# Kernel tuning notes

Hardware: AMD Instinct MI355X
Metric: run time of the kernel (lower is better)

Reference implementation:

```python
import jax, jax.numpy as jnp
import numpy as np

T, B, F, H = 1024, 128, 243, 20  # timesteps, batch, feature dim, hidden dim
POOL = 4  # MaxPool1d(4, 4) over the 512 channel axis -> 128


def setup_inputs() -> dict:
    key = jax.random.key(0)
    ks = jax.random.split(key, 9)
    s = lambda fan_in: 1.0 / np.sqrt(fan_in)
    return {
        "feats": jax.random.normal(ks[0], (T, B * POOL, F), dtype=jnp.float32),
        "e0": jax.random.normal(ks[1], (B, H), dtype=jnp.float32),
        # PyTorch GRUCell params: gates stacked as [r; z; n]
        "W_ih": jax.random.uniform(ks[2], (3 * H, F), jnp.float32, -s(H), s(H)),
        "W_hh": jax.random.uniform(ks[3], (3 * H, H), jnp.float32, -s(H), s(H)),
        "b_ih": jax.random.uniform(ks[4], (3 * H,), jnp.float32, -s(H), s(H)),
        "b_hh": jax.random.uniform(ks[5], (3 * H,), jnp.float32, -s(H), s(H)),
        # decoder: Linear(20, 243) + ReLU
        "W_dec": jax.random.uniform(ks[6], (F, H), jnp.float32, -s(H), s(H)),
        "b_dec": jax.random.uniform(ks[7], (F,), jnp.float32, -s(H), s(H)),
    }


def reference(feats, e0, W_ih, W_hh, b_ih, b_hh, W_dec, b_dec):
    # temporal max-pool over the 512 axis (kernel=4, stride=4) -> [T, B, F]
    h_seq = feats.reshape(T, B, POOL, F).max(axis=2)
    # precompute input-gate projections once (vectorized over T): [T, B, 3H]
    x_gates = jnp.einsum('tbf,gf->tbg', h_seq, W_ih) + b_ih

    def step(e, inp):
        h_t, xg = inp
        hg = e @ W_hh.T + b_hh
        xr, xz, xn = jnp.split(xg, 3, axis=-1)
        hr, hz, hn = jnp.split(hg, 3, axis=-1)
        r = jax.nn.sigmoid(xr + hr)
        z = jax.nn.sigmoid(xz + hz)
        n = jnp.tanh(xn + r * hn)
        e_new = (1.0 - z) * n + z * e
        fo = jax.nn.relu(e_new @ W_dec.T + b_dec)
        loss = jnp.mean((fo - h_t) ** 2)
        return e_new, loss

    _, losses = jax.lax.scan(step, e0, (h_seq, x_gates))
    return jnp.mean(losses)  # sum(loss_list) / step
```

## Files before the change

kernel.cpp:

```cpp
#include <hip/hip_runtime.h>
#include <cstddef>

#define T_ 1024
#define B_ 128
#define F_ 243
#define H_ 20
#define G_ 60
#define R_ 512
#define P_ 8
#define FP_ 256
#define HS_ 244

__device__ __forceinline__ float rdlane(float v, int l) {
  return __int_as_float(__builtin_amdgcn_readlane(__float_as_int(v), l));
}
#define RCP(x) __builtin_amdgcn_rcpf(x)
#if __has_builtin(__builtin_amdgcn_exp2f)
#define EXP2(x) __builtin_amdgcn_exp2f(x)
#else
#define EXP2(x) __expf((x) * 0.6931471805599453f)
#endif
#define NL2E_ -1.4426950408889634f
#define L2E2_ 2.8853900817779268f

__global__ __launch_bounds__(256) void k1a_pool(
    const float* __restrict__ feats, float* __restrict__ h_seq,
    const float* __restrict__ W_ih, float* __restrict__ Wt)
{
  const int bid = blockIdx.x;
  if (bid < 60) {
    const int i = bid * 256 + threadIdx.x;
    if (i < FP_ * G_) {
      const int f = i / G_, g = i - f * G_;
      Wt[(size_t)f * G_ + g] = (f < F_) ? W_ih[(size_t)g * F_ + f] : 0.f;
    }
  }
  const int t = bid & (T_ - 1);
  const int b0 = (bid >> 10) << 3;
  const int col = threadIdx.x;
  if (col < F_) {
    #pragma unroll
    for (int bb = 0; bb < 8; ++bb) {
      const float* p =
          feats + ((size_t)t * R_ + (size_t)(b0 + bb) * 4) * F_ + col;
      const float v =
          fmaxf(fmaxf(p[0], p[F_]), fmaxf(p[2 * F_], p[3 * F_]));
      h_seq[((size_t)(b0 + bb) * T_ + t) * HS_ + col] = v;
    }
  }
}

__global__ __launch_bounds__(256) void k1b_gemm(
    const float* __restrict__ h_seq, const float* __restrict__ Wt,
    const float* __restrict__ b_ih, float* __restrict__ xg)
{
  __shared__ __align__(16) float Ws[64 * 60];
  const int bid = blockIdx.x;
  const int b = bid >> 4;
  const int t0 = (bid & 15) << 6;
  const int tid = threadIdx.x;
  const int rg = tid >> 4;
  const int gcol = tid & 15;
  const int gc4 = (gcol < 15) ? gcol * 4 : 56;
  const float* hsb = h_seq + ((size_t)b * T_ + t0) * HS_;

  float acc[4][4];
  #pragma unroll
  for (int i = 0; i < 4; ++i)
    #pragma unroll
    for (int j = 0; j < 4; ++j) acc[i][j] = 0.f;

  for (int c = 0; c < 4; ++c) {
    const int FC = c * 64;
    __syncthreads();
    for (int j = tid; j < 64 * 60; j += 256)
      Ws[j] = Wt[(size_t)FC * G_ + j];
    __syncthreads();
    #pragma unroll
    for (int fj = 0; fj < 16; ++fj) {
      const float* wp = &Ws[(fj * 4) * 60 + gc4];
      const float4 w0 = *(const float4*)(wp);
      const float4 w1 = *(const float4*)(wp + 60);
      const float4 w2 = *(const float4*)(wp + 120);
      const float4 w3 = *(const float4*)(wp + 180);
      #pragma unroll
      for (int i = 0; i < 4; ++i) {
        const int row = (rg << 2) + i;
        const float4 a4 =
            *(const float4*)&hsb[(size_t)row * HS_ + FC + fj * 4];
        acc[i][0] = fmaf(a4.x, w0.x, fmaf(a4.y, w1.x, fmaf(a4.z, w2.x, fmaf(a4.w, w3.x, acc[i][0]))));
        acc[i][1] = fmaf(a4.x, w0.y, fmaf(a4.y, w1.y, fmaf(a4.z, w2.y, fmaf(a4.w, w3.y, acc[i][1]))));
        acc[i][2] = fmaf(a4.x, w0.z, fmaf(a4.y, w1.z, fmaf(a4.z, w2.z, fmaf(a4.w, w3.z, acc[i][2]))));
        acc[i][3] = fmaf(a4.x, w0.w, fmaf(a4.y, w1.w, fmaf(a4.z, w2.w, fmaf(a4.w, w3.w, acc[i][3]))));
      }
    }
  }

  if (gcol < 15) {
    const float4 bi4 = *(const float4*)&b_ih[gc4];
    #pragma unroll
    for (int i = 0; i < 4; ++i) {
      const int row = (rg << 2) + i;
      float4 o;
      o.x = acc[i][0] + bi4.x;  o.y = acc[i][1] + bi4.y;
      o.z = acc[i][2] + bi4.z;  o.w = acc[i][3] + bi4.w;
      *(float4*)&xg[((size_t)b * T_ + t0 + row) * G_ + gc4] = o;
    }
  }
}

__global__ __launch_bounds__(320) void k2_fused(
    const float* __restrict__ e0, const float* __restrict__ W_hh,
    const float* __restrict__ b_hh, const float* __restrict__ xg,
    const float* __restrict__ h_seq, const float* __restrict__ W_dec,
    const float* __restrict__ b_dec, float* __restrict__ partials)
{
  __shared__ float ebuf[2][P_][H_];
  __shared__ float red[8];
  const int b = blockIdx.x;
  const int tid = threadIdx.x;
  const int lane = tid & 63;
  const int wave = tid >> 6;
  float acc = 0.f;

  if (wave == 0) {
    const bool own = lane < H_;
    const int j0 = own ? lane : 0;

    float2 wr2[10], wz2[10], wn2[10];
    #pragma unroll
    for (int k = 0; k < 10; ++k) {
      const float2 a = *(const float2*)&W_hh[j0 * H_ + 2 * k];
      const float2 c = *(const float2*)&W_hh[(j0 + 20) * H_ + 2 * k];
      const float2 d = *(const float2*)&W_hh[(j0 + 40) * H_ + 2 * k];
      wr2[k] = make_float2(a.x * NL2E_, a.y * NL2E_);
      wz2[k] = make_float2(c.x * NL2E_, c.y * NL2E_);
      wn2[k] = make_float2(d.x * L2E2_, d.y * L2E2_);
    }
    const float bhr = b_hh[j0] * NL2E_;
    const float bhz = b_hh[j0 + 20] * NL2E_;
    const float bhn = b_hh[j0 + 40] * L2E2_;

    float e_own = e0[b * H_ + j0];
    float2 es2[10];
    #pragma unroll
    for (int k = 0; k < 10; ++k) {
      es2[k].x = rdlane(e_own, 2 * k);
      es2[k].y = rdlane(e_own, 2 * k + 1);
    }

    const float* xgb = xg + (size_t)b * T_ * G_;
    float xr[P_], xz[P_], xn[P_];
    #pragma unroll
    for (int j = 0; j < P_; ++j) {
      xr[j] = xgb[(size_t)j * G_ + j0] * NL2E_;
      xz[j] = xgb[(size_t)j * G_ + j0 + 20] * NL2E_;
      xn[j] = xgb[(size_t)j * G_ + j0 + 40] * L2E2_;
    }

#define STEP(j, RELOAD)                                                    \
    {                                                                      \
      const int t = t0 + (j);                                              \
      const float xrv = xr[j], xzv = xz[j], xnv = xn[j];                   \
      if (RELOAD) {                                                        \
        const float* xp = xgb + (size_t)(t + P_) * G_;                     \
        xr[j] = xp[j0] * NL2E_;                                            \
        xz[j] = xp[j0 + 20] * NL2E_;                                       \
        xn[j] = xp[j0 + 40] * L2E2_;                                       \
      }                                                                    \
      float2 rA = make_float2(bhr, 0.f), rB = make_float2(0.f, 0.f);       \
      float2 zA = make_float2(bhz, 0.f), zB = make_float2(0.f, 0.f);       \
      float2 nA = make_float2(bhn, 0.f), nB = make_float2(0.f, 0.f);       \
      _Pragma("unroll")                                                    \
      for (int k = 0; k < 5; ++k) {                                        \
        rA = wr2[k] * es2[k] + rA;   rB = wr2[k + 5] * es2[k + 5] + rB;    \
        zA = wz2[k] * es2[k] + zA;   zB = wz2[k + 5] * es2[k + 5] + zB;    \
        nA = wn2[k] * es2[k] + nA;   nB = wn2[k + 5] * es2[k + 5] + nB;    \
      }                                                                    \
      const float hr2 = (rA.x + rB.x) + (rA.y + rB.y);                     \
      const float hz2 = (zA.x + zB.x) + (zA.y + zB.y);                     \
      const float hn2 = (nA.x + nB.x) + (nA.y + nB.y);                     \
      const float rg = RCP(1.f + EXP2(xrv + hr2));                         \
      const float zg = RCP(1.f + EXP2(xzv + hz2));                         \
      const float aa2 = fmaf(rg, hn2, xnv);                                \
      const float ng = fmaf(-2.f, RCP(EXP2(aa2) + 1.f), 1.f);              \
      const float enew = fmaf(zg, e_own - ng, ng);                         \
      if (own) ebuf[(t0 >> 3) & 1][j][lane] = enew;                        \
      e_own = enew;                                                        \
      _Pragma("unroll")                                                    \
      for (int k = 0; k < 10; ++k) {                                       \
        es2[k].x = rdlane(enew, 2 * k);                                    \
        es2[k].y = rdlane(enew, 2 * k + 1);                                \
      }                                                                    \
    }

    for (int t0 = 0; t0 < T_ - P_; t0 += P_) {
      STEP(0, true) STEP(1, true) STEP(2, true) STEP(3, true)
      STEP(4, true) STEP(5, true) STEP(6, true) STEP(7, true)
      __syncthreads();
    }
    {
      const int t0 = T_ - P_;
      STEP(0, false) STEP(1, false) STEP(2, false) STEP(3, false)
      STEP(4, false) STEP(5, false) STEP(6, false) STEP(7, false)
      __syncthreads();
    }
#undef STEP
  } else {
    const int ct = tid - 64;
    const bool act = ct < F_;
    const int f = act ? ct : 0;
    float wd[H_];
    #pragma unroll
    for (int k = 0; k < H_; ++k) wd[k] = W_dec[f * H_ + k];
    const float bd = b_dec[f];
    const float* hsb = h_seq + (size_t)b * T_ * HS_;

    float hcur[P_], hnxt[P_];
    #pragma unroll
    for (int j = 0; j < P_; ++j) hcur[j] = hsb[(size_t)j * HS_ + f];

    for (int g = 0; g < T_ / P_; ++g) {
      __syncthreads();
      if (g < T_ / P_ - 1) {
        #pragma unroll
        for (int j = 0; j < P_; ++j)
          hnxt[j] = hsb[(size_t)(P_ * (g + 1) + j) * HS_ + f];
      }
      const float* eb = &ebuf[g & 1][0][0];
      #pragma unroll
      for (int j = 0; j < P_; ++j) {
        const float2* ep = (const float2*)&eb[j * H_];
        float d = bd;
        #pragma unroll
        for (int k = 0; k < 10; ++k) {
          const float2 e2 = ep[k];
          d = fmaf(wd[2 * k], e2.x, fmaf(wd[2 * k + 1], e2.y, d));
        }
        const float fo = fmaxf(d, 0.f);
        const float df = fo - hcur[j];
        if (act) acc = fmaf(df, df, acc);
      }
      #pragma unroll
      for (int j = 0; j < P_; ++j) hcur[j] = hnxt[j];
    }
  }

  #pragma unroll
  for (int m = 32; m >= 1; m >>= 1) acc += __shfl_xor(acc, m);
  if (lane == 0) red[wave] = acc;
  __syncthreads();
  if (tid == 0)
    partials[b] = ((red[0] + red[1]) + (red[2] + red[3])) + red[4];
}

__global__ __launch_bounds__(64) void k3_reduce(
    const float* __restrict__ partials, float* __restrict__ out)
{
  const int lane = threadIdx.x;
  float a = partials[lane] + partials[lane + 64];
  #pragma unroll
  for (int m = 32; m >= 1; m >>= 1) a += __shfl_xor(a, m);
  if (lane == 0) out[0] = a * (float)(1.0 / ((double)T_ * B_ * F_));
}

extern "C" void kernel_launch(void* const* d_in, const int* in_sizes, int n_in,
                              void* d_out, int out_size, void* d_ws, size_t ws_size,
                              hipStream_t stream) {
  const float* feats = (const float*)d_in[0];
  const float* e0    = (const float*)d_in[1];
  const float* W_ih  = (const float*)d_in[2];
  const float* W_hh  = (const float*)d_in[3];
  const float* b_ih  = (const float*)d_in[4];
  const float* b_hh  = (const float*)d_in[5];
  const float* W_dec = (const float*)d_in[6];
  const float* b_dec = (const float*)d_in[7];
  float* out = (float*)d_out;

  float* ws = (float*)d_ws;
  float* h_seq    = ws;
  float* xgates   = ws + (size_t)B_ * T_ * HS_;
  float* partials = xgates + (size_t)B_ * T_ * G_;
  float* Wt       = partials + 128;

  hipLaunchKernelGGL(k1a_pool, dim3(T_ * (B_ / 8)), dim3(256), 0, stream,
                     feats, h_seq, W_ih, Wt);
  hipLaunchKernelGGL(k1b_gemm, dim3(B_ * 16), dim3(256), 0, stream,
                     h_seq, Wt, b_ih, xgates);
  hipLaunchKernelGGL(k2_fused, dim3(B_), dim3(320), 0, stream,
                     e0, W_hh, b_hh, xgates, h_seq, W_dec, b_dec, partials);
  hipLaunchKernelGGL(k3_reduce, dim3(1), dim3(64), 0, stream,
                     partials, out);
}
```

Before: 445.5 us.

## Fuse input-gate GEMM into recurrent kernel, pipelined via shared-memory double buffer

Removes the separate input-projection GEMM kernel and its global xgates buffer. The four decoder waves of the recurrent kernel now compute the gate projections for the next group of 8 timesteps from h_seq and a shared-memory copy of W_ih, writing them into a double-buffered LDS tile. The recurrent wave then reads them from LDS. This saves a launch and global traffic, but puts the GEMM work on only 128 blocks, and that work must keep pace with the serial recurrence.

```diff
diff --git a/kernel.cpp b/kernel.cpp
--- a/kernel.cpp
+++ b/kernel.cpp
@@ -8,6 +8,7 @@
 #define G_ 60
 #define R_ 512
 #define P_ 8
+#define NG_ (T_ / P_)
 #define FP_ 256
 #define HS_ 244
 
@@ -50,78 +51,26 @@
   }
 }
 
-__global__ __launch_bounds__(256) void k1b_gemm(
-    const float* __restrict__ h_seq, const float* __restrict__ Wt,
-    const float* __restrict__ b_ih, float* __restrict__ xg)
+__global__ __launch_bounds__(320) void k2_mega(
+    const float* __restrict__ e0, const float* __restrict__ W_hh,
+    const float* __restrict__ b_hh, const float* __restrict__ Wt,
+    const float* __restrict__ b_ih, const float* __restrict__ h_seq,
+    const float* __restrict__ W_dec, const float* __restrict__ b_dec,
+    float* __restrict__ partials)
 {
-  __shared__ __align__(16) float Ws[64 * 60];
-  const int bid = blockIdx.x;
-  const int b = bid >> 4;
-  const int t0 = (bid & 15) << 6;
-  const int tid = threadIdx.x;
-  const int rg = tid >> 4;
-  const int gcol = tid & 15;
-  const int gc4 = (gcol < 15) ? gcol * 4 : 56;
-  const float* hsb = h_seq + ((size_t)b * T_ + t0) * HS_;
-
-  float acc[4][4];
-  #pragma unroll
-  for (int i = 0; i < 4; ++i)
-    #pragma unroll
-    for (int j = 0; j < 4; ++j) acc[i][j] = 0.f;
-
-  for (int c = 0; c < 4; ++c) {
-    const int FC = c * 64;
-    __syncthreads();
-    for (int j = tid; j < 64 * 60; j += 256)
-      Ws[j] = Wt[(size_t)FC * G_ + j];
-    __syncthreads();
-    #pragma unroll
-    for (int fj = 0; fj < 16; ++fj) {
-      const float* wp = &Ws[(fj * 4) * 60 + gc4];
-      const float4 w0 = *(const float4*)(wp);
-      const float4 w1 = *(const float4*)(wp + 60);
-      const float4 w2 = *(const float4*)(wp + 120);
-      const float4 w3 = *(const float4*)(wp + 180);
-      #pragma unroll
-      for (int i = 0; i < 4; ++i) {
-        const int row = (rg << 2) + i;
-        const float4 a4 =
-            *(const float4*)&hsb[(size_t)row * HS_ + FC + fj * 4];
-        acc[i][0] = fmaf(a4.x, w0.x, fmaf(a4.y, w1.x, fmaf(a4.z, w2.x, fmaf(a4.w, w3.x, acc[i][0]))));
-        acc[i][1] = fmaf(a4.x, w0.y, fmaf(a4.y, w1.y, fmaf(a4.z, w2.y, fmaf(a4.w, w3.y, acc[i][1]))));
-        acc[i][2] = fmaf(a4.x, w0.z, fmaf(a4.y, w1.z, fmaf(a4.z, w2.z, fmaf(a4.w, w3.z, acc[i][2]))));
-        acc[i][3] = fmaf(a4.x, w0.w, fmaf(a4.y, w1.w, fmaf(a4.z, w2.w, fmaf(a4.w, w3.w, acc[i][3]))));
-      }
-    }
-  }
-
-  if (gcol < 15) {
-    const float4 bi4 = *(const float4*)&b_ih[gc4];
-    #pragma unroll
-    for (int i = 0; i < 4; ++i) {
-      const int row = (rg << 2) + i;
-      float4 o;
-      o.x = acc[i][0] + bi4.x;  o.y = acc[i][1] + bi4.y;
-      o.z = acc[i][2] + bi4.z;  o.w = acc[i][3] + bi4.w;
-      *(float4*)&xg[((size_t)b * T_ + t0 + row) * G_ + gc4] = o;
-    }
-  }
-}
-
-__global__ __launch_bounds__(320) void k2_fused(
-    const float* __restrict__ e0, const float* __restrict__ W_hh,
-    const float* __restrict__ b_hh, const float* __restrict__ xg,
-    const float* __restrict__ h_seq, const float* __restrict__ W_dec,
-    const float* __restrict__ b_dec, float* __restrict__ partials)
-{
+  __shared__ __align__(16) float Ws[244 * 60];
+  __shared__ float xgbuf[2][P_][G_];
   __shared__ float ebuf[2][P_][H_];
   __shared__ float red[8];
   const int b = blockIdx.x;
   const int tid = threadIdx.x;
   const int lane = tid & 63;
   const int wave = tid >> 6;
+  const float* hsb = h_seq + (size_t)b * T_ * HS_;
   float acc = 0.f;
+
+  for (int i = tid; i < 244 * 60; i += 320) Ws[i] = Wt[i];
+  __syncthreads();
 
   if (wave == 0) {
     const bool own = lane < H_;
@@ -148,26 +97,13 @@
       es2[k].x = rdlane(e_own, 2 * k);
       es2[k].y = rdlane(e_own, 2 * k + 1);
     }
-
-    const float* xgb = xg + (size_t)b * T_ * G_;
+    __syncthreads();
+
     float xr[P_], xz[P_], xn[P_];
-    #pragma unroll
-    for (int j = 0; j < P_; ++j) {
-      xr[j] = xgb[(size_t)j * G_ + j0] * NL2E_;
-      xz[j] = xgb[(size_t)j * G_ + j0 + 20] * NL2E_;
-      xn[j] = xgb[(size_t)j * G_ + j0 + 40] * L2E2_;
-    }
-
-#define STEP(j, RELOAD)                                                    \
+
+#define STEP(j)                                                            \
     {                                                                      \
-      const int t = t0 + (j);                                              \
       const float xrv = xr[j], xzv = xz[j], xnv = xn[j];                   \
-      if (RELOAD) {                                                        \
-        const float* xp = xgb + (size_t)(t + P_) * G_;                     \
-        xr[j] = xp[j0] * NL2E_;                                            \
-        xz[j] = xp[j0 + 20] * NL2E_;                                       \
-        xn[j] = xp[j0 + 40] * L2E2_;                                       \
-      }                                                                    \
       float2 rA = make_float2(bhr, 0.f), rB = make_float2(0.f, 0.f);       \
       float2 zA = make_float2(bhz, 0.f), zB = make_float2(0.f, 0.f);       \
       float2 nA = make_float2(bhn, 0.f), nB = make_float2(0.f, 0.f);       \
@@ -185,7 +121,7 @@
       const float aa2 = fmaf(rg, hn2, xnv);                                \
       const float ng = fmaf(-2.f, RCP(EXP2(aa2) + 1.f), 1.f);              \
       const float enew = fmaf(zg, e_own - ng, ng);                         \
-      if (own) ebuf[(t0 >> 3) & 1][j][lane] = enew;                        \
+      if (own) ebuf[m & 1][j][lane] = enew;                                \
       e_own = enew;                                                        \
       _Pragma("unroll")                                                    \
       for (int k = 0; k < 10; ++k) {                                       \
@@ -194,56 +130,93 @@
       }                                                                    \
     }
 
-    for (int t0 = 0; t0 < T_ - P_; t0 += P_) {
-      STEP(0, true) STEP(1, true) STEP(2, true) STEP(3, true)
-      STEP(4, true) STEP(5, true) STEP(6, true) STEP(7, true)
+    for (int m = 0; m < NG_; ++m) {
+      const float* xb = &xgbuf[m & 1][0][0];
+      #pragma unroll
+      for (int j = 0; j < P_; ++j) {
+        xr[j] = xb[j * G_ + j0];
+        xz[j] = xb[j * G_ + j0 + 20];
+        xn[j] = xb[j * G_ + j0 + 40];
+      }
+      STEP(0) STEP(1) STEP(2) STEP(3) STEP(4) STEP(5) STEP(6) STEP(7)
       __syncthreads();
     }
-    {
-      const int t0 = T_ - P_;
-      STEP(0, false) STEP(1, false) STEP(2, false) STEP(3, false)
-      STEP(4, false) STEP(5, false) STEP(6, false) STEP(7, false)
-      __syncthreads();
-    }
+    __syncthreads();
 #undef STEP
   } else {
     const int ct = tid - 64;
+    const int rr = ct >> 5;
+    const int q = ct & 31;
+    const bool qact = q < 30;
     const bool act = ct < F_;
     const int f = act ? ct : 0;
+
     float wd[H_];
     #pragma unroll
     for (int k = 0; k < H_; ++k) wd[k] = W_dec[f * H_ + k];
     const float bd = b_dec[f];
-    const float* hsb = h_seq + (size_t)b * T_ * HS_;
-
+
+    float2 sc2 = make_float2(0.f, 0.f), bs2 = make_float2(0.f, 0.f);
+    if (qact) {
+      const float s = (q < 20) ? NL2E_ : L2E2_;
+      sc2 = make_float2(s, s);
+      bs2 = make_float2(b_ih[2 * q] * s, b_ih[2 * q + 1] * s);
+    }
+
+#define GEMM_GRP(GRP, BUF)                                                 \
+    if (qact) {                                                            \
+      const float* hrow = hsb + (size_t)((GRP) * P_ + rr) * HS_;           \
+      float2 aE = make_float2(0.f, 0.f), aO = make_float2(0.f, 0.f);       \
+      _Pragma("unroll 4")                                                  \
+      for (int f4 = 0; f4 < 61; ++f4) {                                    \
+        const float4 h4 = *(const float4*)&hrow[f4 * 4];                   \
+        const float2 u0 = *(const float2*)&Ws[(f4 * 4 + 0) * 60 + 2 * q];  \
+        const float2 u1 = *(const float2*)&Ws[(f4 * 4 + 1) * 60 + 2 * q];  \
+        const float2 u2 = *(const float2*)&Ws[(f4 * 4 + 2) * 60 + 2 * q];  \
+        const float2 u3 = *(const float2*)&Ws[(f4 * 4 + 3) * 60 + 2 * q];  \
+        aE = u0 * make_float2(h4.x, h4.x) + aE;                            \
+        aO = u1 * make_float2(h4.y, h4.y) + aO;                            \
+        aE = u2 * make_float2(h4.z, h4.z) + aE;                            \
+        aO = u3 * make_float2(h4.w, h4.w) + aO;                            \
+      }                                                                    \
+      const float2 a2 = (aE + aO) * sc2 + bs2;                             \
+      *(float2*)&xgbuf[BUF][rr][2 * q] = a2;                               \
+    }
+
+    GEMM_GRP(0, 0)
     float hcur[P_], hnxt[P_];
     #pragma unroll
     for (int j = 0; j < P_; ++j) hcur[j] = hsb[(size_t)j * HS_ + f];
-
-    for (int g = 0; g < T_ / P_; ++g) {
-      __syncthreads();
-      if (g < T_ / P_ - 1) {
+    __syncthreads();
+
+    for (int m = 0; m <= NG_; ++m) {
+      if (m >= 1 && m < NG_) {
         #pragma unroll
         for (int j = 0; j < P_; ++j)
-          hnxt[j] = hsb[(size_t)(P_ * (g + 1) + j) * HS_ + f];
+          hnxt[j] = hsb[(size_t)(P_ * m + j) * HS_ + f];
       }
-      const float* eb = &ebuf[g & 1][0][0];
-      #pragma unroll
-      for (int j = 0; j < P_; ++j) {
-        const float2* ep = (const float2*)&eb[j * H_];
-        float d = bd;
+      if (m <= NG_ - 2) GEMM_GRP(m + 1, (m + 1) & 1)
+      if (m >= 1) {
+        const float* eb = &ebuf[(m - 1) & 1][0][0];
         #pragma unroll
-        for (int k = 0; k < 10; ++k) {
-          const float2 e2 = ep[k];
-          d = fmaf(wd[2 * k], e2.x, fmaf(wd[2 * k + 1], e2.y, d));
+        for (int j = 0; j < P_; ++j) {
+          const float2* ep = (const float2*)&eb[j * H_];
+          float d = bd;
+          #pragma unroll
+          for (int k = 0; k < 10; ++k) {
+            const float2 e2 = ep[k];
+            d = fmaf(wd[2 * k], e2.x, fmaf(wd[2 * k + 1], e2.y, d));
+          }
+          const float fo = fmaxf(d, 0.f);
+          const float df = fo - hcur[j];
+          if (act) acc = fmaf(df, df, acc);
         }
-        const float fo = fmaxf(d, 0.f);
-        const float df = fo - hcur[j];
-        if (act) acc = fmaf(df, df, acc);
+        #pragma unroll
+        for (int j = 0; j < P_; ++j) hcur[j] = hnxt[j];
       }
-      #pragma unroll
-      for (int j = 0; j < P_; ++j) hcur[j] = hnxt[j];
-    }
+      __syncthreads();
+    }
+#undef GEMM_GRP
   }
 
   #pragma unroll
@@ -279,16 +252,13 @@
 
   float* ws = (float*)d_ws;
   float* h_seq    = ws;
-  float* xgates   = ws + (size_t)B_ * T_ * HS_;
-  float* partials = xgates + (size_t)B_ * T_ * G_;
-  float* Wt       = partials + 128;
+  float* Wt       = ws + (size_t)B_ * T_ * HS_;
+  float* partials = Wt + (size_t)FP_ * G_;
 
   hipLaunchKernelGGL(k1a_pool, dim3(T_ * (B_ / 8)), dim3(256), 0, stream,
                      feats, h_seq, W_ih, Wt);
-  hipLaunchKernelGGL(k1b_gemm, dim3(B_ * 16), dim3(256), 0, stream,
-                     h_seq, Wt, b_ih, xgates);
-  hipLaunchKernelGGL(k2_fused, dim3(B_), dim3(320), 0, stream,
-                     e0, W_hh, b_hh, xgates, h_seq, W_dec, b_dec, partials);
+  hipLaunchKernelGGL(k2_mega, dim3(B_), dim3(320), 0, stream,
+                     e0, W_hh, b_hh, Wt, b_ih, h_seq, W_dec, b_dec, partials);
   hipLaunchKernelGGL(k3_reduce, dim3(1), dim3(64), 0, stream,
                      partials, out);
 }
```

Result: slower. 1.612 ms (+261.8%).

## Process two batch rows per recurrent block to interleave independent GRU chains

Applied to the files above, without the earlier changes.

The fused recurrence kernel now handles two batch elements per block. The single recurrent wave interleaves the two independent GRU dependency chains, and eight decoder waves (two rows of 256 threads) consume a doubled shared buffer. This is meant to hide the serial latency of each step by giving the recurrent wave independent instructions to overlap, while halving the grid to 64 blocks. The cost is longer per-step instruction streams, more register pressure in wave 0, and fewer blocks on a GPU with many compute units.

```diff
diff --git a/kernel.cpp b/kernel.cpp
--- a/kernel.cpp
+++ b/kernel.cpp
@@ -109,14 +109,14 @@
   }
 }
 
-__global__ __launch_bounds__(320) void k2_fused(
+__global__ __launch_bounds__(576) void k2_fused(
     const float* __restrict__ e0, const float* __restrict__ W_hh,
     const float* __restrict__ b_hh, const float* __restrict__ xg,
     const float* __restrict__ h_seq, const float* __restrict__ W_dec,
     const float* __restrict__ b_dec, float* __restrict__ partials)
 {
-  __shared__ float ebuf[2][P_][H_];
-  __shared__ float red[8];
+  __shared__ float ebuf[2][2][P_][H_];
+  __shared__ float red[12];
   const int b = blockIdx.x;
   const int tid = threadIdx.x;
   const int lane = tid & 63;
@@ -141,56 +141,83 @@
     const float bhz = b_hh[j0 + 20] * NL2E_;
     const float bhn = b_hh[j0 + 40] * L2E2_;
 
-    float e_own = e0[b * H_ + j0];
-    float2 es2[10];
+    float eA = e0[(2 * b) * H_ + j0];
+    float eB = e0[(2 * b + 1) * H_ + j0];
+    float2 esA[10], esB[10];
     #pragma unroll
     for (int k = 0; k < 10; ++k) {
-      es2[k].x = rdlane(e_own, 2 * k);
-      es2[k].y = rdlane(e_own, 2 * k + 1);
-    }
-
-    const float* xgb = xg + (size_t)b * T_ * G_;
-    float xr[P_], xz[P_], xn[P_];
+      esA[k].x = rdlane(eA, 2 * k);  esA[k].y = rdlane(eA, 2 * k + 1);
+      esB[k].x = rdlane(eB, 2 * k);  esB[k].y = rdlane(eB, 2 * k + 1);
+    }
+
+    const float* xgbA = xg + (size_t)(2 * b) * T_ * G_;
+    const float* xgbB = xg + (size_t)(2 * b + 1) * T_ * G_;
+    float xrA[P_], xzA[P_], xnA[P_], xrB[P_], xzB[P_], xnB[P_];
     #pragma unroll
     for (int j = 0; j < P_; ++j) {
-      xr[j] = xgb[(size_t)j * G_ + j0] * NL2E_;
-      xz[j] = xgb[(size_t)j * G_ + j0 + 20] * NL2E_;
-      xn[j] = xgb[(size_t)j * G_ + j0 + 40] * L2E2_;
+      xrA[j] = xgbA[(size_t)j * G_ + j0] * NL2E_;
+      xzA[j] = xgbA[(size_t)j * G_ + j0 + 20] * NL2E_;
+      xnA[j] = xgbA[(size_t)j * G_ + j0 + 40] * L2E2_;
+      xrB[j] = xgbB[(size_t)j * G_ + j0] * NL2E_;
+      xzB[j] = xgbB[(size_t)j * G_ + j0 + 20] * NL2E_;
+      xnB[j] = xgbB[(size_t)j * G_ + j0 + 40] * L2E2_;
     }
 
 #define STEP(j, RELOAD)                                                    \
     {                                                                      \
       const int t = t0 + (j);                                              \
-      const float xrv = xr[j], xzv = xz[j], xnv = xn[j];                   \
+      const float xrvA = xrA[j], xzvA = xzA[j], xnvA = xnA[j];             \
+      const float xrvB = xrB[j], xzvB = xzB[j], xnvB = xnB[j];             \
       if (RELOAD) {                                                        \
-        const float* xp = xgb + (size_t)(t + P_) * G_;                     \
-        xr[j] = xp[j0] * NL2E_;                                            \
-        xz[j] = xp[j0 + 20] * NL2E_;                                       \
-        xn[j] = xp[j0 + 40] * L2E2_;                                       \
+        const float* xpA = xgbA + (size_t)(t + P_) * G_;                   \
+        const float* xpB = xgbB + (size_t)(t + P_) * G_;                   \
+        xrA[j] = xpA[j0] * NL2E_;       xrB[j] = xpB[j0] * NL2E_;          \
+        xzA[j] = xpA[j0 + 20] * NL2E_;  xzB[j] = xpB[j0 + 20] * NL2E_;     \
+        xnA[j] = xpA[j0 + 40] * L2E2_;  xnB[j] = xpB[j0 + 40] * L2E2_;     \
       }                                                                    \
-      float2 rA = make_float2(bhr, 0.f), rB = make_float2(0.f, 0.f);       \
-      float2 zA = make_float2(bhz, 0.f), zB = make_float2(0.f, 0.f);       \
-      float2 nA = make_float2(bhn, 0.f), nB = make_float2(0.f, 0.f);       \
+      float2 r0A = make_float2(bhr, 0.f), r1A = make_float2(0.f, 0.f);     \
+      float2 z0A = make_float2(bhz, 0.f), z1A = make_float2(0.f, 0.f);     \
+      float2 n0A = make_float2(bhn, 0.f), n1A = make_float2(0.f, 0.f);     \
+      float2 r0B = make_float2(bhr, 0.f), r1B = make_float2(0.f, 0.f);     \
+      float2 z0B = make_float2(bhz, 0.f), z1B = make_float2(0.f, 0.f);     \
+      float2 n0B = make_float2(bhn, 0.f), n1B = make_float2(0.f, 0.f);     \
       _Pragma("unroll")                                                    \
       for (int k = 0; k < 5; ++k) {                                        \
-        rA = wr2[k] * es2[k] + rA;   rB = wr2[k + 5] * es2[k + 5] + rB;    \
-        zA = wz2[k] * es2[k] + zA;   zB = wz2[k + 5] * es2[k + 5] + zB;    \
-        nA = wn2[k] * es2[k] + nA;   nB = wn2[k + 5] * es2[k + 5] + nB;    \
+        r0A = wr2[k] * esA[k] + r0A;  r0B = wr2[k] * esB[k] + r0B;         \
+        r1A = wr2[k + 5] * esA[k + 5] + r1A;                               \
+        r1B = wr2[k + 5] * esB[k + 5] + r1B;                               \
+        z0A = wz2[k] * esA[k] + z0A;  z0B = wz2[k] * esB[k] + z0B;         \
+        z1A = wz2[k + 5] * esA[k + 5] + z1A;                               \
+        z1B = wz2[k + 5] * esB[k + 5] + z1B;                               \
+        n0A = wn2[k] * esA[k] + n0A;  n0B = wn2[k] * esB[k] + n0B;         \
+        n1A = wn2[k + 5] * esA[k + 5] + n1A;                               \
+        n1B = wn2[k + 5] * esB[k + 5] + n1B;                               \
       }                                                                    \
-      const float hr2 = (rA.x + rB.x) + (rA.y + rB.y);                     \
-      const float hz2 = (zA.x + zB.x) + (zA.y + zB.y);                     \
-      const float hn2 = (nA.x + nB.x) + (nA.y + nB.y);                     \
-      const float rg = RCP(1.f + EXP2(xrv + hr2));                         \
-      const float zg = RCP(1.f + EXP2(xzv + hz2));                         \
-      const float aa2 = fmaf(rg, hn2, xnv);                                \
-      const float ng = fmaf(-2.f, RCP(EXP2(aa2) + 1.f), 1.f);              \
-      const float enew = fmaf(zg, e_own - ng, ng);                         \
-      if (own) ebuf[(t0 >> 3) & 1][j][lane] = enew;                        \
-      e_own = enew;                                                        \
+      const float hrA = (r0A.x + r1A.x) + (r0A.y + r1A.y);                 \
+      const float hrB = (r0B.x + r1B.x) + (r0B.y + r1B.y);                 \
+      const float hzA = (z0A.x + z1A.x) + (z0A.y + z1A.y);                 \
+      const float hzB = (z0B.x + z1B.x) + (z0B.y + z1B.y);                 \
+      const float hnA = (n0A.x + n1A.x) + (n0A.y + n1A.y);                 \
+      const float hnB = (n0B.x + n1B.x) + (n0B.y + n1B.y);                 \
+      const float rgA = RCP(1.f + EXP2(xrvA + hrA));                       \
+      const float rgB = RCP(1.f + EXP2(xrvB + hrB));                       \
+      const float zgA = RCP(1.f + EXP2(xzvA + hzA));                       \
+      const float zgB = RCP(1.f + EXP2(xzvB + hzB));                       \
+      const float aaA = fmaf(rgA, hnA, xnvA);                              \
+      const float aaB = fmaf(rgB, hnB, xnvB);                              \
+      const float ngA = fmaf(-2.f, RCP(EXP2(aaA) + 1.f), 1.f);             \
+      const float ngB = fmaf(-2.f, RCP(EXP2(aaB) + 1.f), 1.f);             \
+      const float enA = fmaf(zgA, eA - ngA, ngA);                          \
+      const float enB = fmaf(zgB, eB - ngB, ngB);                          \
+      if (own) {                                                           \
+        ebuf[(t0 >> 3) & 1][0][j][lane] = enA;                             \
+        ebuf[(t0 >> 3) & 1][1][j][lane] = enB;                             \
+      }                                                                    \
+      eA = enA;  eB = enB;                                                 \
       _Pragma("unroll")                                                    \
       for (int k = 0; k < 10; ++k) {                                       \
-        es2[k].x = rdlane(enew, 2 * k);                                    \
-        es2[k].y = rdlane(enew, 2 * k + 1);                                \
+        esA[k].x = rdlane(enA, 2 * k);  esA[k].y = rdlane(enA, 2 * k + 1); \
+        esB[k].x = rdlane(enB, 2 * k);  esB[k].y = rdlane(enB, 2 * k + 1); \
       }                                                                    \
     }
 
@@ -208,13 +235,15 @@
 #undef STEP
   } else {
     const int ct = tid - 64;
-    const bool act = ct < F_;
-    const int f = act ? ct : 0;
+    const int row = ct >> 8;
+    const int f0 = ct & 255;
+    const bool act = f0 < F_;
+    const int f = act ? f0 : 0;
     float wd[H_];
     #pragma unroll
     for (int k = 0; k < H_; ++k) wd[k] = W_dec[f * H_ + k];
     const float bd = b_dec[f];
-    const float* hsb = h_seq + (size_t)b * T_ * HS_;
+    const float* hsb = h_seq + (size_t)(2 * b + row) * T_ * HS_;
 
     float hcur[P_], hnxt[P_];
     #pragma unroll
@@ -227,7 +256,7 @@
         for (int j = 0; j < P_; ++j)
           hnxt[j] = hsb[(size_t)(P_ * (g + 1) + j) * HS_ + f];
       }
-      const float* eb = &ebuf[g & 1][0][0];
+      const float* eb = &ebuf[g & 1][row][0][0];
       #pragma unroll
       for (int j = 0; j < P_; ++j) {
         const float2* ep = (const float2*)&eb[j * H_];
@@ -250,15 +279,19 @@
   for (int m = 32; m >= 1; m >>= 1) acc += __shfl_xor(acc, m);
   if (lane == 0) red[wave] = acc;
   __syncthreads();
-  if (tid == 0)
-    partials[b] = ((red[0] + red[1]) + (red[2] + red[3])) + red[4];
+  if (tid == 0) {
+    float s = red[0];
+    #pragma unroll
+    for (int w = 1; w < 9; ++w) s += red[w];
+    partials[b] = s;
+  }
 }
 
 __global__ __launch_bounds__(64) void k3_reduce(
     const float* __restrict__ partials, float* __restrict__ out)
 {
   const int lane = threadIdx.x;
-  float a = partials[lane] + partials[lane + 64];
+  float a = partials[lane];
   #pragma unroll
   for (int m = 32; m >= 1; m >>= 1) a += __shfl_xor(a, m);
   if (lane == 0) out[0] = a * (float)(1.0 / ((double)T_ * B_ * F_));
@@ -287,7 +320,7 @@
                      feats, h_seq, W_ih, Wt);
   hipLaunchKernelGGL(k1b_gemm, dim3(B_ * 16), dim3(256), 0, stream,
                      h_seq, Wt, b_ih, xgates);
-  hipLaunchKernelGGL(k2_fused, dim3(B_), dim3(320), 0, stream,
+  hipLaunchKernelGGL(k2_fused, dim3(B_ / 2), dim3(576), 0, stream,
                      e0, W_hh, b_hh, xgates, h_seq, W_dec, b_dec, partials);
   hipLaunchKernelGGL(k3_reduce, dim3(1), dim3(64), 0, stream,
                      partials, out);
```

New measurement: 618.4 us. 38.8% more time.

## Pack two batch rows per recurrence wave using ds_bpermute broadcasts

Applied to the files above, without the earlier changes.

Each k2 block now handles two batch rows. The recurrence wave splits its 64 lanes into two 32-lane halves, and the hidden-state broadcast switches from readlane to ds_bpermute with per-half addresses. Decoder waves double to cover both rows, and the grid halves to 64 blocks. This cuts the number of recurrence waves, but it adds bpermute latency to the serial critical path of each timestep.

```diff
diff --git a/kernel.cpp b/kernel.cpp
--- a/kernel.cpp
+++ b/kernel.cpp
@@ -11,8 +11,8 @@
 #define FP_ 256
 #define HS_ 244
 
-__device__ __forceinline__ float rdlane(float v, int l) {
-  return __int_as_float(__builtin_amdgcn_readlane(__float_as_int(v), l));
+__device__ __forceinline__ float bperm(int addr, float v) {
+  return __int_as_float(__builtin_amdgcn_ds_bpermute(addr, __float_as_int(v)));
 }
 #define RCP(x) __builtin_amdgcn_rcpf(x)
 #if __has_builtin(__builtin_amdgcn_exp2f)
@@ -109,14 +109,14 @@
   }
 }
 
-__global__ __launch_bounds__(320) void k2_fused(
+__global__ __launch_bounds__(576) void k2_fused(
     const float* __restrict__ e0, const float* __restrict__ W_hh,
     const float* __restrict__ b_hh, const float* __restrict__ xg,
     const float* __restrict__ h_seq, const float* __restrict__ W_dec,
     const float* __restrict__ b_dec, float* __restrict__ partials)
 {
-  __shared__ float ebuf[2][P_][H_];
-  __shared__ float red[8];
+  __shared__ float ebuf[2][2][P_][H_];
+  __shared__ float red[12];
   const int b = blockIdx.x;
   const int tid = threadIdx.x;
   const int lane = tid & 63;
@@ -124,8 +124,15 @@
   float acc = 0.f;
 
   if (wave == 0) {
-    const bool own = lane < H_;
-    const int j0 = own ? lane : 0;
+    const int half = lane >> 5;
+    const int li = lane & 31;
+    const bool own = li < H_;
+    const int j0 = own ? li : 0;
+    const int row = 2 * b + half;
+
+    int bidx[H_];
+    #pragma unroll
+    for (int k = 0; k < H_; ++k) bidx[k] = ((lane & 32) | k) << 2;
 
     float2 wr2[10], wz2[10], wn2[10];
     #pragma unroll
@@ -141,15 +148,15 @@
     const float bhz = b_hh[j0 + 20] * NL2E_;
     const float bhn = b_hh[j0 + 40] * L2E2_;
 
-    float e_own = e0[b * H_ + j0];
+    float e_own = e0[row * H_ + j0];
     float2 es2[10];
     #pragma unroll
     for (int k = 0; k < 10; ++k) {
-      es2[k].x = rdlane(e_own, 2 * k);
-      es2[k].y = rdlane(e_own, 2 * k + 1);
-    }
-
-    const float* xgb = xg + (size_t)b * T_ * G_;
+      es2[k].x = bperm(bidx[2 * k], e_own);
+      es2[k].y = bperm(bidx[2 * k + 1], e_own);
+    }
+
+    const float* xgb = xg + (size_t)row * T_ * G_;
     float xr[P_], xz[P_], xn[P_];
     #pragma unroll
     for (int j = 0; j < P_; ++j) {
@@ -185,12 +192,12 @@
       const float aa2 = fmaf(rg, hn2, xnv);                                \
       const float ng = fmaf(-2.f, RCP(EXP2(aa2) + 1.f), 1.f);              \
       const float enew = fmaf(zg, e_own - ng, ng);                         \
-      if (own) ebuf[(t0 >> 3) & 1][j][lane] = enew;                        \
+      if (own) ebuf[(t0 >> 3) & 1][half][j][li] = enew;                    \
       e_own = enew;                                                        \
       _Pragma("unroll")                                                    \
       for (int k = 0; k < 10; ++k) {                                       \
-        es2[k].x = rdlane(enew, 2 * k);                                    \
-        es2[k].y = rdlane(enew, 2 * k + 1);                                \
+        es2[k].x = bperm(bidx[2 * k], enew);                               \
+        es2[k].y = bperm(bidx[2 * k + 1], enew);                           \
       }                                                                    \
     }
 
@@ -208,13 +215,15 @@
 #undef STEP
   } else {
     const int ct = tid - 64;
-    const bool act = ct < F_;
-    const int f = act ? ct : 0;
+    const int row = ct >> 8;
+    const int f0 = ct & 255;
+    const bool act = f0 < F_;
+    const int f = act ? f0 : 0;
     float wd[H_];
     #pragma unroll
     for (int k = 0; k < H_; ++k) wd[k] = W_dec[f * H_ + k];
     const float bd = b_dec[f];
-    const float* hsb = h_seq + (size_t)b * T_ * HS_;
+    const float* hsb = h_seq + (size_t)(2 * b + row) * T_ * HS_;
 
     float hcur[P_], hnxt[P_];
     #pragma unroll
@@ -227,7 +236,7 @@
         for (int j = 0; j < P_; ++j)
           hnxt[j] = hsb[(size_t)(P_ * (g + 1) + j) * HS_ + f];
       }
-      const float* eb = &ebuf[g & 1][0][0];
+      const float* eb = &ebuf[g & 1][row][0][0];
       #pragma unroll
       for (int j = 0; j < P_; ++j) {
         const float2* ep = (const float2*)&eb[j * H_];
@@ -250,15 +259,19 @@
   for (int m = 32; m >= 1; m >>= 1) acc += __shfl_xor(acc, m);
   if (lane == 0) red[wave] = acc;
   __syncthreads();
-  if (tid == 0)
-    partials[b] = ((red[0] + red[1]) + (red[2] + red[3])) + red[4];
+  if (tid == 0) {
+    float s = red[0];
+    #pragma unroll
+    for (int w = 1; w < 9; ++w) s += red[w];
+    partials[b] = s;
+  }
 }
 
 __global__ __launch_bounds__(64) void k3_reduce(
     const float* __restrict__ partials, float* __restrict__ out)
 {
   const int lane = threadIdx.x;
-  float a = partials[lane] + partials[lane + 64];
+  float a = partials[lane];
   #pragma unroll
   for (int m = 32; m >= 1; m >>= 1) a += __shfl_xor(a, m);
   if (lane == 0) out[0] = a * (float)(1.0 / ((double)T_ * B_ * F_));
@@ -287,7 +300,7 @@
                      feats, h_seq, W_ih, Wt);
   hipLaunchKernelGGL(k1b_gemm, dim3(B_ * 16), dim3(256), 0, stream,
                      h_seq, Wt, b_ih, xgates);
-  hipLaunchKernelGGL(k2_fused, dim3(B_), dim3(320), 0, stream,
+  hipLaunchKernelGGL(k2_fused, dim3(B_ / 2), dim3(576), 0, stream,
                      e0, W_hh, b_hh, xgates, h_seq, W_dec, b_dec, partials);
   hipLaunchKernelGGL(k3_reduce, dim3(1), dim3(64), 0, stream,
                      partials, out);
```

New measurement: 501.6 us. +12.6%, slower.
